# Optimization experiments

Hardware: AMD Instinct MI355X
Metric: run time of the kernel (lower is better)

Reference implementation:

```python
import jax, jax.numpy as jnp
import numpy as np

NUM_HEADS = 16
D_ATT = 64


def setup_inputs() -> dict:
    key = jax.random.key(0)
    ks = jax.random.split(key, 7)
    b, n, hd = 4, 2048, NUM_HEADS * 64  # input last dim = num_heads * per-head embed_dim
    Q_vec = jax.random.normal(ks[0], (b, n, hd), dtype=jnp.float32)
    K_vec = jax.random.normal(ks[1], (b, n, hd), dtype=jnp.float32)
    V_vec = jax.random.normal(ks[2], (b, n, hd), dtype=jnp.float32)
    # torch Linear weights: [out_features, in_features] = [d_attention, per_head_dim]
    W_Q = jax.random.normal(ks[3], (D_ATT, 64), dtype=jnp.float32) * 0.02
    W_K = jax.random.normal(ks[4], (D_ATT, 64), dtype=jnp.float32) * 0.02
    W_V = jax.random.normal(ks[5], (D_ATT, 64), dtype=jnp.float32) * 0.02
    mask = jax.random.bernoulli(ks[6], p=0.9, shape=(b, n))  # bool [b, n]
    return {"Q_vec": Q_vec, "K_vec": K_vec, "V_vec": V_vec,
            "W_Q": W_Q, "W_K": W_K, "W_V": W_V, "mask": mask}


def reference(Q_vec, K_vec, V_vec, W_Q, W_K, W_V, mask):
    b, n, _ = Q_vec.shape
    h = NUM_HEADS
    scaling = 1.0 / np.sqrt(D_ATT).astype(np.float32)

    def split_heads(x):  # b n (h d) -> b h n d
        return x.reshape(b, n, h, -1).transpose(0, 2, 1, 3)

    # Linear applied per-head (weights are [out, in]; y = x @ W^T)
    q = split_heads(Q_vec) @ W_Q.T  # [b,h,n,D_ATT]
    k = split_heads(K_vec) @ W_K.T
    v = split_heads(V_vec) @ W_V.T

    dots = jnp.einsum('bhid,bhjd->bhij', q, k) * scaling  # [b,h,n,n]
    pair_mask = mask[:, None, :] & mask[:, :, None]       # [b,n,n]
    mask_value = -jnp.finfo(dots.dtype).max
    dots = jnp.where(pair_mask[:, None, :, :], dots, mask_value)
    attn = jax.nn.softmax(dots, axis=-1)
    out = jnp.einsum('bhij,bhjd->bhid', attn, v)          # [b,h,n,D_ATT]
    return out.transpose(0, 2, 1, 3).reshape(b, n, h * D_ATT)
```

## Files before the change

### kernel.cpp

```cpp
#include <hip/hip_runtime.h>

#define B_  4
#define N_  2048
#define H_  16
#define HD_ 1024

typedef short  bf16x8 __attribute__((ext_vector_type(8)));
typedef short  bf16x4 __attribute__((ext_vector_type(4)));
typedef float  f32x4  __attribute__((ext_vector_type(4)));

static __device__ __forceinline__ unsigned short f2bf(float f) {
    unsigned int u = __builtin_bit_cast(unsigned int, f);
    u += 0x7FFFu + ((u >> 16) & 1u);
    return (unsigned short)(u >> 16);
}

static __device__ __forceinline__ unsigned rne_hi(float f) {
    unsigned u = __builtin_bit_cast(unsigned, f);
    return u + 0x7FFFu + ((u >> 16) & 1u);
}
static __device__ __forceinline__ unsigned f2bf2pack(float lo, float hi) {
    return __builtin_amdgcn_perm(rne_hi(hi), rne_hi(lo), 0x07060302u);
}

__global__ __launch_bounds__(256) void proj_kernel(
    const float* __restrict__ Qv, const float* __restrict__ Kv,
    const float* __restrict__ Vv, const float* __restrict__ WQ,
    const float* __restrict__ WK, const float* __restrict__ WV,
    unsigned short* __restrict__ qs, unsigned short* __restrict__ ks,
    unsigned short* __restrict__ vt)
{
    __shared__ __align__(16) unsigned short xb[64][72];
    __shared__ __align__(16) unsigned short Wb[64][72];
    __shared__ __align__(16) unsigned short sb[64][72];

    const int tid  = threadIdx.x;
    const int wq   = tid >> 6;
    const int lane = tid & 63;
    const int l15  = lane & 15;
    const int quad = lane >> 4;

    const int i0 = blockIdx.x * 64;
    const int h  = blockIdx.y;
    const int bz = blockIdx.z;
    const int b  = bz / 3;
    const int p  = bz - b * 3;

    const size_t inbase = ((size_t)b * N_ + i0) * HD_ + h * 64;
    const size_t bh     = (size_t)b * H_ + h;

    const float* W   = (p == 0) ? WQ : (p == 1) ? WK : WV;
    const float* inp = ((p == 0) ? Qv : (p == 1) ? Kv : Vv) + inbase;

    for (int v = tid; v < 1024; v += 256) {
        int tok = v >> 4, c4 = (v & 15) * 4;
        float4 f = *reinterpret_cast<const float4*>(inp + (size_t)tok * HD_ + c4);
        uint2 u;
        u.x = f2bf2pack(f.x, f.y);
        u.y = f2bf2pack(f.z, f.w);
        *reinterpret_cast<uint2*>(&xb[tok][c4]) = u;
        float4 g = *reinterpret_cast<const float4*>(W + (size_t)v * 4);
        uint2 w2;
        w2.x = f2bf2pack(g.x, g.y);
        w2.y = f2bf2pack(g.z, g.w);
        *reinterpret_cast<uint2*>(&Wb[tok][c4]) = w2;
    }
    __syncthreads();

    bf16x8 ax[2];
    #pragma unroll
    for (int kh = 0; kh < 2; ++kh)
        ax[kh] = *reinterpret_cast<const bf16x8*>(&xb[wq * 16 + l15][kh * 32 + quad * 8]);

    f32x4 C[4];
    #pragma unroll
    for (int t = 0; t < 4; ++t) {
        C[t] = f32x4{0.f, 0.f, 0.f, 0.f};
        #pragma unroll
        for (int kh = 0; kh < 2; ++kh) {
            bf16x8 bw = *reinterpret_cast<const bf16x8*>(&Wb[t * 16 + l15][kh * 32 + quad * 8]);
            C[t] = __builtin_amdgcn_mfma_f32_16x16x32_bf16(ax[kh], bw, C[t], 0, 0, 0);
        }
    }

    if (p < 2) {
        const float scl = (p == 0) ? 0.180336880f : 1.f;
        #pragma unroll
        for (int t = 0; t < 4; ++t)
            #pragma unroll
            for (int r = 0; r < 4; ++r)
                sb[wq * 16 + quad * 4 + r][t * 16 + l15] = f2bf(C[t][r] * scl);
        __syncthreads();
        unsigned short* dst = ((p == 0) ? qs : ks) + ((size_t)bh * N_ + i0) * 64;
        for (int v = tid; v < 512; v += 256) {
            int row = v >> 3, c0 = (v & 7) * 8;
            *reinterpret_cast<uint4*>(dst + (size_t)row * 64 + c0) =
                *reinterpret_cast<const uint4*>(&sb[row][c0]);
        }
    } else {
        #pragma unroll
        for (int t = 0; t < 4; ++t) {
            uint2 u;
            u.x = f2bf2pack(C[t][0], C[t][1]);
            u.y = f2bf2pack(C[t][2], C[t][3]);
            *reinterpret_cast<uint2*>(&sb[t * 16 + l15][wq * 16 + quad * 4]) = u;
        }
        __syncthreads();
        unsigned short* vdst = vt + (size_t)bh * 64 * N_ + i0;
        for (int v = tid; v < 512; v += 256) {
            int d = v >> 3, c0 = (v & 7) * 8;
            *reinterpret_cast<uint4*>(vdst + (size_t)d * N_ + c0) =
                *reinterpret_cast<const uint4*>(&sb[d][c0]);
        }
    }
}

__global__ __launch_bounds__(256, 2) void attn_kernel(
    const unsigned short* __restrict__ qs, const unsigned short* __restrict__ ks,
    const unsigned short* __restrict__ vt, const int* __restrict__ maskp,
    float* __restrict__ out)
{
    __shared__ __align__(16) unsigned short Ks[64][72];
    __shared__ __align__(16) unsigned short Vt[64][68];
    __shared__ float kb[64];

    const int tid  = threadIdx.x;
    const int w    = tid >> 6;
    const int lane = tid & 63;
    const int l15  = lane & 15;
    const int quad = lane >> 4;

    const int i0 = blockIdx.x * 256;
    const int bh = blockIdx.y;
    const int b  = bh >> 4;
    const int h  = bh & 15;
    const int qrow0 = i0 + w * 64;

    bf16x8 aq[4][2];
    float  qm[4];
    #pragma unroll
    for (int rt = 0; rt < 4; ++rt) {
        const unsigned short* qrow = qs + ((size_t)bh * N_ + qrow0 + rt * 16 + l15) * 64;
        aq[rt][0] = *reinterpret_cast<const bf16x8*>(qrow + quad * 8);
        aq[rt][1] = *reinterpret_cast<const bf16x8*>(qrow + 32 + quad * 8);
        qm[rt] = maskp[b * N_ + qrow0 + rt * 16 + l15] ? 1.f : 0.f;
    }

    bf16x8 aones;
    #pragma unroll
    for (int j = 0; j < 8; ++j) aones[j] = (short)0x3F80;

    f32x4 O[4][4];
    f32x4 L[4];
    #pragma unroll
    for (int rt = 0; rt < 4; ++rt) {
        L[rt] = f32x4{0.f, 0.f, 0.f, 0.f};
        #pragma unroll
        for (int c = 0; c < 4; ++c) O[rt][c] = f32x4{0.f, 0.f, 0.f, 0.f};
    }

    const unsigned short* kbase = ks + (size_t)bh * N_ * 64;
    const unsigned short* vbase = vt + (size_t)bh * 64 * N_;

    for (int kv0 = 0; kv0 < N_; kv0 += 64) {
        __syncthreads();
        #pragma unroll
        for (int it = 0; it < 2; ++it) {
            int idx = tid + it * 256;
            int r = idx >> 3, g = idx & 7;
            *reinterpret_cast<uint4*>(&Ks[r][g * 8]) =
                *reinterpret_cast<const uint4*>(kbase + (size_t)(kv0 + r) * 64 + g * 8);
        }
        #pragma unroll
        for (int it = 0; it < 4; ++it) {
            int idx = tid + it * 256;
            int r = idx >> 4, g2 = idx & 15;
            *reinterpret_cast<uint2*>(&Vt[r][g2 * 4]) =
                *reinterpret_cast<const uint2*>(vbase + (size_t)r * N_ + kv0 + g2 * 4);
        }
        if (tid < 64) kb[tid] = maskp[b * N_ + kv0 + tid] ? 0.f : -1e30f;
        __syncthreads();

        bf16x8 ak[4][2];
        #pragma unroll
        for (int ct = 0; ct < 4; ++ct)
            #pragma unroll
            for (int kh = 0; kh < 2; ++kh)
                ak[ct][kh] = *reinterpret_cast<const bf16x8*>(&Ks[ct * 16 + l15][kh * 32 + quad * 8]);

        bf16x8 av[4][2];
        #pragma unroll
        for (int ct = 0; ct < 4; ++ct)
            #pragma unroll
            for (int kh = 0; kh < 2; ++kh) {
                bf16x4 lo = *reinterpret_cast<const bf16x4*>(&Vt[ct * 16 + l15][kh * 32 + quad * 4]);
                bf16x4 hi = *reinterpret_cast<const bf16x4*>(&Vt[ct * 16 + l15][kh * 32 + 16 + quad * 4]);
                av[ct][kh] = bf16x8{lo[0], lo[1], lo[2], lo[3], hi[0], hi[1], hi[2], hi[3]};
            }

        f32x4 kbv[4];
        #pragma unroll
        for (int ct = 0; ct < 4; ++ct)
            kbv[ct] = *reinterpret_cast<const f32x4*>(&kb[ct * 16 + quad * 4]);

        #pragma unroll
        for (int rt = 0; rt < 4; ++rt) {
            f32x4 S[4];
            #pragma unroll
            for (int ct = 0; ct < 4; ++ct) {
                S[ct] = f32x4{0.f, 0.f, 0.f, 0.f};
                #pragma unroll
                for (int kh = 0; kh < 2; ++kh)
                    S[ct] = __builtin_amdgcn_mfma_f32_16x16x32_bf16(ak[ct][kh], aq[rt][kh], S[ct], 0, 0, 0);
            }
            unsigned pk[4][2];
            #pragma unroll
            for (int ct = 0; ct < 4; ++ct) {
                float e0 = __builtin_amdgcn_exp2f((S[ct][0] + kbv[ct][0]) * qm[rt]);
                float e1 = __builtin_amdgcn_exp2f((S[ct][1] + kbv[ct][1]) * qm[rt]);
                float e2 = __builtin_amdgcn_exp2f((S[ct][2] + kbv[ct][2]) * qm[rt]);
                float e3 = __builtin_amdgcn_exp2f((S[ct][3] + kbv[ct][3]) * qm[rt]);
                pk[ct][0] = f2bf2pack(e0, e1);
                pk[ct][1] = f2bf2pack(e2, e3);
            }
            bf16x8 ap[2];
            #pragma unroll
            for (int kh = 0; kh < 2; ++kh) {
                uint4 u = uint4{pk[2 * kh][0], pk[2 * kh][1], pk[2 * kh + 1][0], pk[2 * kh + 1][1]};
                ap[kh] = __builtin_bit_cast(bf16x8, u);
            }
            #pragma unroll
            for (int kh = 0; kh < 2; ++kh)
                L[rt] = __builtin_amdgcn_mfma_f32_16x16x32_bf16(aones, ap[kh], L[rt], 0, 0, 0);
            #pragma unroll
            for (int ct = 0; ct < 4; ++ct)
                #pragma unroll
                for (int kh = 0; kh < 2; ++kh)
                    O[rt][ct] = __builtin_amdgcn_mfma_f32_16x16x32_bf16(av[ct][kh], ap[kh], O[rt][ct], 0, 0, 0);
        }
    }

    #pragma unroll
    for (int rt = 0; rt < 4; ++rt) {
        float inv = 1.f / L[rt][0];
        float* orow = out + ((size_t)b * N_ + qrow0 + rt * 16 + l15) * HD_ + h * 64 + quad * 4;
        #pragma unroll
        for (int ct = 0; ct < 4; ++ct)
            #pragma unroll
            for (int r = 0; r < 4; ++r)
                orow[ct * 16 + r] = O[rt][ct][r] * inv;
    }
}

extern "C" void kernel_launch(void* const* d_in, const int* in_sizes, int n_in,
                              void* d_out, int out_size, void* d_ws, size_t ws_size,
                              hipStream_t stream)
{
    const float* Qv  = (const float*)d_in[0];
    const float* Kv  = (const float*)d_in[1];
    const float* Vv  = (const float*)d_in[2];
    const float* WQ  = (const float*)d_in[3];
    const float* WK  = (const float*)d_in[4];
    const float* WV  = (const float*)d_in[5];
    const int*   msk = (const int*)d_in[6];
    float* out = (float*)d_out;

    const size_t per = (size_t)B_ * H_ * N_ * 64;
    unsigned short* qsb = (unsigned short*)d_ws;
    unsigned short* ksb = qsb + per;
    unsigned short* vtb = ksb + per;

    proj_kernel<<<dim3(N_ / 64, H_, B_ * 3), 256, 0, stream>>>(Qv, Kv, Vv, WQ, WK, WV, qsb, ksb, vtb);
    attn_kernel<<<dim3(N_ / 256, B_ * H_), 256, 0, stream>>>(qsb, ksb, vtb, msk, out);
}
```

Measured before the change: 243.9 us.

## Double-buffer K/V tiles via register prefetch, add MFMA priority hints

```diff
diff --git a/kernel.cpp b/kernel.cpp
--- a/kernel.cpp
+++ b/kernel.cpp
@@ -32,7 +32,7 @@
 {
     __shared__ __align__(16) unsigned short xb[64][72];
     __shared__ __align__(16) unsigned short Wb[64][72];
-    __shared__ __align__(16) unsigned short sb[64][72];
+    unsigned short (*sb)[72] = xb;
 
     const int tid  = threadIdx.x;
     const int wq   = tid >> 6;
@@ -83,6 +83,8 @@
         }
     }
 
+    __syncthreads();
+
     if (p < 2) {
         const float scl = (p == 0) ? 0.180336880f : 1.f;
         #pragma unroll
@@ -120,9 +122,9 @@
     const unsigned short* __restrict__ vt, const int* __restrict__ maskp,
     float* __restrict__ out)
 {
-    __shared__ __align__(16) unsigned short Ks[64][72];
-    __shared__ __align__(16) unsigned short Vt[64][68];
-    __shared__ float kb[64];
+    __shared__ __align__(16) unsigned short Ks[2][64][72];
+    __shared__ __align__(16) unsigned short Vt[2][64][68];
+    __shared__ __align__(16) float kb[2][64];
 
     const int tid  = threadIdx.x;
     const int w    = tid >> 6;
@@ -162,50 +164,64 @@
     const unsigned short* kbase = ks + (size_t)bh * N_ * 64;
     const unsigned short* vbase = vt + (size_t)bh * 64 * N_;
 
-    for (int kv0 = 0; kv0 < N_; kv0 += 64) {
-        __syncthreads();
+    #pragma unroll
+    for (int it = 0; it < 2; ++it) {
+        int idx = tid + it * 256, r = idx >> 3, g = idx & 7;
+        *reinterpret_cast<uint4*>(&Ks[0][r][g * 8]) =
+            *reinterpret_cast<const uint4*>(kbase + (size_t)r * 64 + g * 8);
+    }
+    #pragma unroll
+    for (int it = 0; it < 4; ++it) {
+        int idx = tid + it * 256, r = idx >> 4, g2 = idx & 15;
+        *reinterpret_cast<uint2*>(&Vt[0][r][g2 * 4]) =
+            *reinterpret_cast<const uint2*>(vbase + (size_t)r * N_ + g2 * 4);
+    }
+    if (tid < 64) kb[0][tid] = maskp[b * N_ + tid] ? 0.f : -1e30f;
+    __syncthreads();
+
+    auto tile_step = [&](int kv0, int cur, int nb) __attribute__((always_inline)) {
+        const int kvn = (kv0 + 64) & (N_ - 1);
+        uint4 kreg[2];
         #pragma unroll
         for (int it = 0; it < 2; ++it) {
-            int idx = tid + it * 256;
-            int r = idx >> 3, g = idx & 7;
-            *reinterpret_cast<uint4*>(&Ks[r][g * 8]) =
-                *reinterpret_cast<const uint4*>(kbase + (size_t)(kv0 + r) * 64 + g * 8);
-        }
+            int idx = tid + it * 256, r = idx >> 3, g = idx & 7;
+            kreg[it] = *reinterpret_cast<const uint4*>(kbase + (size_t)(kvn + r) * 64 + g * 8);
+        }
+        uint2 vreg[4];
         #pragma unroll
         for (int it = 0; it < 4; ++it) {
-            int idx = tid + it * 256;
-            int r = idx >> 4, g2 = idx & 15;
-            *reinterpret_cast<uint2*>(&Vt[r][g2 * 4]) =
-                *reinterpret_cast<const uint2*>(vbase + (size_t)r * N_ + kv0 + g2 * 4);
-        }
-        if (tid < 64) kb[tid] = maskp[b * N_ + kv0 + tid] ? 0.f : -1e30f;
-        __syncthreads();
+            int idx = tid + it * 256, r = idx >> 4, g2 = idx & 15;
+            vreg[it] = *reinterpret_cast<const uint2*>(vbase + (size_t)r * N_ + kvn + g2 * 4);
+        }
+        float kmr = 0.f;
+        if (tid < 64) kmr = maskp[b * N_ + kvn + tid] ? 0.f : -1e30f;
 
         bf16x8 ak[4][2];
         #pragma unroll
         for (int ct = 0; ct < 4; ++ct)
             #pragma unroll
             for (int kh = 0; kh < 2; ++kh)
-                ak[ct][kh] = *reinterpret_cast<const bf16x8*>(&Ks[ct * 16 + l15][kh * 32 + quad * 8]);
+                ak[ct][kh] = *reinterpret_cast<const bf16x8*>(&Ks[cur][ct * 16 + l15][kh * 32 + quad * 8]);
 
         bf16x8 av[4][2];
         #pragma unroll
         for (int ct = 0; ct < 4; ++ct)
             #pragma unroll
             for (int kh = 0; kh < 2; ++kh) {
-                bf16x4 lo = *reinterpret_cast<const bf16x4*>(&Vt[ct * 16 + l15][kh * 32 + quad * 4]);
-                bf16x4 hi = *reinterpret_cast<const bf16x4*>(&Vt[ct * 16 + l15][kh * 32 + 16 + quad * 4]);
+                bf16x4 lo = *reinterpret_cast<const bf16x4*>(&Vt[cur][ct * 16 + l15][kh * 32 + quad * 4]);
+                bf16x4 hi = *reinterpret_cast<const bf16x4*>(&Vt[cur][ct * 16 + l15][kh * 32 + 16 + quad * 4]);
                 av[ct][kh] = bf16x8{lo[0], lo[1], lo[2], lo[3], hi[0], hi[1], hi[2], hi[3]};
             }
 
         f32x4 kbv[4];
         #pragma unroll
         for (int ct = 0; ct < 4; ++ct)
-            kbv[ct] = *reinterpret_cast<const f32x4*>(&kb[ct * 16 + quad * 4]);
+            kbv[ct] = *reinterpret_cast<const f32x4*>(&kb[cur][ct * 16 + quad * 4]);
 
         #pragma unroll
         for (int rt = 0; rt < 4; ++rt) {
             f32x4 S[4];
+            __builtin_amdgcn_s_setprio(1);
             #pragma unroll
             for (int ct = 0; ct < 4; ++ct) {
                 S[ct] = f32x4{0.f, 0.f, 0.f, 0.f};
@@ -213,6 +229,7 @@
                 for (int kh = 0; kh < 2; ++kh)
                     S[ct] = __builtin_amdgcn_mfma_f32_16x16x32_bf16(ak[ct][kh], aq[rt][kh], S[ct], 0, 0, 0);
             }
+            __builtin_amdgcn_s_setprio(0);
             unsigned pk[4][2];
             #pragma unroll
             for (int ct = 0; ct < 4; ++ct) {
@@ -229,6 +246,7 @@
                 uint4 u = uint4{pk[2 * kh][0], pk[2 * kh][1], pk[2 * kh + 1][0], pk[2 * kh + 1][1]};
                 ap[kh] = __builtin_bit_cast(bf16x8, u);
             }
+            __builtin_amdgcn_s_setprio(1);
             #pragma unroll
             for (int kh = 0; kh < 2; ++kh)
                 L[rt] = __builtin_amdgcn_mfma_f32_16x16x32_bf16(aones, ap[kh], L[rt], 0, 0, 0);
@@ -237,7 +255,26 @@
                 #pragma unroll
                 for (int kh = 0; kh < 2; ++kh)
                     O[rt][ct] = __builtin_amdgcn_mfma_f32_16x16x32_bf16(av[ct][kh], ap[kh], O[rt][ct], 0, 0, 0);
-        }
+            __builtin_amdgcn_s_setprio(0);
+        }
+
+        #pragma unroll
+        for (int it = 0; it < 2; ++it) {
+            int idx = tid + it * 256, r = idx >> 3, g = idx & 7;
+            *reinterpret_cast<uint4*>(&Ks[nb][r][g * 8]) = kreg[it];
+        }
+        #pragma unroll
+        for (int it = 0; it < 4; ++it) {
+            int idx = tid + it * 256, r = idx >> 4, g2 = idx & 15;
+            *reinterpret_cast<uint2*>(&Vt[nb][r][g2 * 4]) = vreg[it];
+        }
+        if (tid < 64) kb[nb][tid] = kmr;
+        __syncthreads();
+    };
+
+    for (int kv0 = 0; kv0 < N_; kv0 += 128) {
+        tile_step(kv0, 0, 1);
+        tile_step(kv0 + 64, 1, 0);
     }
 
     #pragma unroll
```

After: 264.6 us. 8.5% more time.
